# Performance work log

Measured on AMD Instinct MI355X. Metric: run time of the kernel, lower is better.

The kernel has to match this reference:

```python
import jax, jax.numpy as jnp
import numpy as np

B, N, D, H, K = 16, 256, 64, 64, 2  # batch, nodes, d_in, d_hidden, top_k


def setup_inputs() -> dict:
    key = jax.random.key(0)
    k0, k1, k2 = jax.random.split(key, 3)
    O = jax.random.normal(k0, (B, N, D), dtype=jnp.float32)
    # PairwiseFeaturizer.proj: Linear(4*D, H) -> ReLU -> Linear(H, 1)
    W1 = jax.random.normal(k1, (4 * D, H), dtype=jnp.float32) / np.sqrt(4 * D).astype(np.float32)
    b1 = jnp.zeros((H,), dtype=jnp.float32)
    W2 = jax.random.normal(k2, (H, 1), dtype=jnp.float32) / np.sqrt(H).astype(np.float32)
    b2 = jnp.zeros((1,), dtype=jnp.float32)
    return {"O": O, "W1": W1, "b1": b1, "W2": W2, "b2": b2}


def reference(O, W1, b1, W2, b2):
    Bn, Nn, d = O.shape
    ii, jj = jnp.triu_indices(Nn, k=1)  # all undirected pairs i<j, M = N(N-1)/2
    Oi = O[:, ii, :]  # (B, M, d) gather
    Oj = O[:, jj, :]  # (B, M, d) gather
    feats = jnp.concatenate([Oi, Oj, jnp.abs(Oi - Oj), Oi * Oj], axis=-1)  # (B, M, 4d)
    h = jax.nn.relu(jnp.einsum('bmf,fh->bmh', feats, W1) + b1)
    Q = (jnp.einsum('bmh,ho->bmo', h, W2) + b2)[..., 0]  # (B, M)
    # greedy top-k selection mask (eps -> 0 limit of select_pairs)
    idx = jax.lax.top_k(Q, K)[1]  # (B, K)
    mask = jnp.zeros(Q.shape, dtype=bool).at[jnp.arange(Q.shape[0])[:, None], idx].set(True)
    return Q, mask
```

## Files before the change

kernel.cpp:

```cpp
#include <hip/hip_runtime.h>
#include <math.h>

#define Bn 16
#define Nn 256
#define Mm (Nn*(Nn-1)/2)
#define CHUNK 4080

typedef __attribute__((ext_vector_type(8))) short bf16x8;
typedef __attribute__((ext_vector_type(4))) short short4v;
typedef __attribute__((ext_vector_type(4))) float f32x4;

typedef union { bf16x8 v; short s[8]; __bf16 h[8]; } F8;
typedef union { short4v v; __bf16 h[4]; } F4;

#define MFMA(acc, a, b) \
  acc = __builtin_amdgcn_mfma_f32_16x16x32_bf16((a), (b), (acc), 0, 0, 0)

__device__ __forceinline__ void top2_update(float v, int m,
    float& v1, int& i1, float& v2, int& i2)
{
  bool c1 = (v > v1) || (v == v1 && m < i1);
  bool c2 = (v > v2) || (v == v2 && m < i2);
  float nv2 = c1 ? v1 : (c2 ? v : v2);
  int   ni2 = c1 ? i1 : (c2 ? m : i2);
  v1 = c1 ? v : v1;  i1 = c1 ? m : i1;
  v2 = nv2;          i2 = ni2;
}

__global__ __launch_bounds__(256) void prep_w1t(
    const float* __restrict__ W1, unsigned short* __restrict__ wtg)
{
  const int h = blockIdx.x;
  const int k = threadIdx.x;
  __bf16 b = (__bf16)W1[k * 64 + h];
  wtg[h * 256 + k] = *(unsigned short*)&b;
}

__global__ __launch_bounds__(256) void prep_ac(
    const float* __restrict__ O, const float* __restrict__ b1,
    const unsigned short* __restrict__ wtg,
    unsigned short* __restrict__ obg, float* __restrict__ Ag,
    unsigned short* __restrict__ Cgb)
{
  __shared__ __align__(16) unsigned short s_ob[64][72];
  const int t = threadIdx.x, l = t & 63, wv = t >> 6;
  const int lo = l & 15, g = l >> 4;
  const int b = blockIdx.x >> 2, rt = blockIdx.x & 3;
  const int r0 = rt * 64;
  const float* Ob = O + ((size_t)b * Nn + r0) * 64;

  #pragma unroll
  for (int p = 0; p < 4; ++p) {
    int v = t + p * 256;
    int r = v >> 4, c4 = (v & 15) * 4;
    float4 x = ((const float4*)Ob)[v];
    F4 pk; pk.h[0] = (__bf16)x.x; pk.h[1] = (__bf16)x.y;
           pk.h[2] = (__bf16)x.z; pk.h[3] = (__bf16)x.w;
    *(short4v*)&s_ob[r][c4] = pk.v;
    *(short4v*)&obg[((size_t)b * Nn + r0 + r) * 64 + c4] = pk.v;
  }
  __syncthreads();

  F8 aop[2];
  #pragma unroll
  for (int ks = 0; ks < 2; ++ks)
    aop[ks].v = *(const bf16x8*)&s_ob[wv * 16 + lo][ks * 32 + g * 8];

  #pragma unroll
  for (int half = 0; half < 2; ++half) {
    #pragma unroll
    for (int nf = 0; nf < 4; ++nf) {
      f32x4 ac = {0.f, 0.f, 0.f, 0.f};
      #pragma unroll
      for (int ks = 0; ks < 2; ++ks) {
        F8 bop; bop.v = *(const bf16x8*)&wtg[(nf * 16 + lo) * 256 + half * 64 + ks * 32 + g * 8];
        MFMA(ac, aop[ks].v, bop.v);
      }
      const int h = nf * 16 + lo;
      if (half == 0) {
        float bb = b1[h];
        #pragma unroll
        for (int r = 0; r < 4; ++r)
          Ag[((size_t)b * Nn + r0 + wv * 16 + g * 4 + r) * 64 + h] = ac[r] + bb;
      } else {
        #pragma unroll
        for (int r = 0; r < 4; ++r) {
          __bf16 cb = (__bf16)ac[r];
          Cgb[((size_t)b * Nn + r0 + wv * 16 + g * 4 + r) * 64 + h] = *(unsigned short*)&cb;
        }
      }
    }
  }
}

__global__ __launch_bounds__(256, 2) void pair_kernel(
    const unsigned short* __restrict__ obg,
    const float* __restrict__ Ag,
    const unsigned short* __restrict__ Cgb,
    const float* __restrict__ W2,
    const float* __restrict__ b2,
    const unsigned short* __restrict__ wtg,
    float* __restrict__ Q,
    float* __restrict__ cand)
{
  __shared__ __align__(16) unsigned short s_wt[64][136];
  __shared__ __align__(16) unsigned short s_oi[16][72];
  __shared__ __align__(16) unsigned short s_oj[32][72];
  __shared__ float s_A [16][68];
  __shared__ float s_q [16][36];
  __shared__ float s_w2[64];
  __shared__ float s_red[4][4];

  const int t  = threadIdx.x;
  const int l  = t & 63, wv = t >> 6;
  const int lo = l & 15, g = l >> 4;

  const int blk    = blockIdx.x;
  const int within = blk >> 3;
  const int batch  = (blk & 7) * 2 + within / 72;
  int tl           = within % 72;
  int a = 0;
  while (tl >= 8 - (a >> 1)) { tl -= 8 - (a >> 1); ++a; }
  const int c   = (a >> 1) + tl;
  const int ti0 = a * 16, tj0 = c * 32;

  {
    const int h = t >> 2, kq = (t & 3) * 32;
    #pragma unroll
    for (int q = 0; q < 4; ++q) {
      *(bf16x8*)&s_wt[h][kq + q * 8] =
          *(const bf16x8*)&wtg[h * 256 + 128 + kq + q * 8];
    }
  }
  {
    int r = t >> 4, c4 = (t & 15) * 4;
    *(short4v*)&s_oi[r][c4] =
        *(const short4v*)&obg[((size_t)batch * Nn + ti0 + r) * 64 + c4];
    *(f32x4*)&s_A[r][c4] =
        *(const f32x4*)&Ag[((size_t)batch * Nn + ti0 + r) * 64 + c4];
    #pragma unroll
    for (int p = 0; p < 2; ++p) {
      int v = t + p * 256;
      int rj = v >> 4, cj = (v & 15) * 4;
      *(short4v*)&s_oj[rj][cj] =
          *(const short4v*)&obg[((size_t)batch * Nn + tj0 + rj) * 64 + cj];
    }
    if (t < 64) s_w2[t] = W2[t];
  }
  __syncthreads();

  F8 bfr[4][4];
  #pragma unroll
  for (int ks = 0; ks < 4; ++ks)
    #pragma unroll
    for (int nf = 0; nf < 4; ++nf)
      bfr[ks][nf].v = *(const bf16x8*)&s_wt[nf * 16 + lo][ks * 32 + g * 8];

  F8 ojb[2][2];
  #pragma unroll
  for (int jh = 0; jh < 2; ++jh) {
    ojb[jh][0].v = *(const bf16x8*)&s_oj[jh * 16 + lo][g * 8];
    ojb[jh][1].v = *(const bf16x8*)&s_oj[jh * 16 + lo][32 + g * 8];
  }
  F4 cinb[2][4];
  #pragma unroll
  for (int jh = 0; jh < 2; ++jh)
    #pragma unroll
    for (int nf = 0; nf < 4; ++nf)
      cinb[jh][nf].v = *(const short4v*)
          &Cgb[((size_t)batch * Nn + tj0 + jh * 16 + lo) * 64 + nf * 16 + g * 4];

  for (int ii = 0; ii < 4; ++ii) {
    const int iL = wv * 4 + ii;

    float oiv[16];
    {
      F8 u0, u1;
      u0.v = *(const bf16x8*)&s_oi[iL][g * 8];
      u1.v = *(const bf16x8*)&s_oi[iL][32 + g * 8];
      #pragma unroll
      for (int e = 0; e < 8; ++e) {
        oiv[e]     = (float)u0.h[e];
        oiv[8 + e] = (float)u1.h[e];
      }
    }
    f32x4 as4[4];
    #pragma unroll
    for (int nf = 0; nf < 4; ++nf)
      as4[nf] = *(const f32x4*)&s_A[iL][nf * 16 + g * 4];

    #pragma unroll
    for (int jh = 0; jh < 2; ++jh) {
      F8 fb0, fb1, fb2, fb3;
      #pragma unroll
      for (int e = 0; e < 8; ++e) {
        float p0 = (float)ojb[jh][0].h[e];
        float p1 = (float)ojb[jh][1].h[e];
        fb0.h[e] = (__bf16)fabsf(oiv[e]     - p0);
        fb1.h[e] = (__bf16)fabsf(oiv[8 + e] - p1);
        fb2.h[e] = (__bf16)(oiv[e]     * p0);
        fb3.h[e] = (__bf16)(oiv[8 + e] * p1);
      }

      f32x4 acc[4] = { as4[0], as4[1], as4[2], as4[3] };
      #pragma unroll
      for (int nf = 0; nf < 4; ++nf) {
        MFMA(acc[nf], bfr[0][nf].v, fb0.v);
        MFMA(acc[nf], bfr[1][nf].v, fb1.v);
        MFMA(acc[nf], bfr[2][nf].v, fb2.v);
        MFMA(acc[nf], bfr[3][nf].v, fb3.v);
      }

      float part = 0.f;
      #pragma unroll
      for (int nf = 0; nf < 4; ++nf) {
        #pragma unroll
        for (int r = 0; r < 4; ++r) {
          float z = acc[nf][r] + (float)cinb[jh][nf].h[r];
          part = fmaf(fmaxf(z, 0.f), s_w2[nf * 16 + g * 4 + r], part);
        }
      }
      part += __shfl_xor(part, 16);
      part += __shfl_xor(part, 32);
      if (g == 0) s_q[iL][jh * 16 + lo] = part;
    }
  }
  __syncthreads();

  {
    const float b2v = b2[0];
    const int e0 = t * 2;
    const int row = e0 >> 5, col0 = e0 & 31;
    const int i = ti0 + row;
    float v1 = -INFINITY, v2 = -INFINITY;
    int   i1 = 0x7fffffff, i2 = 0x7fffffff;
    const int mbase = i * (Nn - 1) - (i * (i - 1)) / 2 - i - 1;
    #pragma unroll
    for (int e = 0; e < 2; ++e) {
      const int col = col0 + e;
      const int j = tj0 + col;
      const float qv = s_q[row][col] + b2v;
      if (j > i) {
        const int m = mbase + j;
        Q[(size_t)batch * Mm + m] = qv;
        top2_update(qv, m, v1, i1, v2, i2);
      }
    }
    #pragma unroll
    for (int s = 1; s < 64; s <<= 1) {
      float u1 = __shfl_xor(v1, s); int j1 = __shfl_xor(i1, s);
      float u2 = __shfl_xor(v2, s); int j2 = __shfl_xor(i2, s);
      top2_update(u1, j1, v1, i1, v2, i2);
      top2_update(u2, j2, v1, i1, v2, i2);
    }
    if (l == 0) {
      s_red[wv][0] = v1; s_red[wv][1] = __int_as_float(i1);
      s_red[wv][2] = v2; s_red[wv][3] = __int_as_float(i2);
    }
    __syncthreads();
    if (t == 0) {
      float a1 = s_red[0][0]; int x1 = __float_as_int(s_red[0][1]);
      float a2 = s_red[0][2]; int x2 = __float_as_int(s_red[0][3]);
      #pragma unroll
      for (int e = 1; e < 4; ++e) {
        top2_update(s_red[e][0], __float_as_int(s_red[e][1]), a1, x1, a2, x2);
        top2_update(s_red[e][2], __float_as_int(s_red[e][3]), a1, x1, a2, x2);
      }
      float* cp = cand + ((size_t)batch * 72 + within % 72) * 4;
      cp[0] = a1; cp[1] = __int_as_float(x1);
      cp[2] = a2; cp[3] = __int_as_float(x2);
    }
  }
}

__global__ __launch_bounds__(256) void rankmask_kernel(
    const float* __restrict__ O, const float* __restrict__ W1,
    const float* __restrict__ b1, const float* __restrict__ W2,
    const float* __restrict__ cand, float* __restrict__ mask)
{
  const int b   = blockIdx.x >> 3;
  const int cch = blockIdx.x & 7;
  const int t   = threadIdx.x;
  const int wv  = t >> 6, h = t & 63;
  __shared__ float s_cv[144];
  __shared__ int   s_ci[144];
  __shared__ int   s_m[8];
  __shared__ int   s_ij[8][2];
  __shared__ float s_or[8][2][64];
  __shared__ float s_qe[8];
  __shared__ int   s_k0, s_k1;

  if (t < 144) {
    const float* cp = cand + (size_t)(b * 72 + (t >> 1)) * 4;
    s_cv[t] = cp[(t & 1) * 2];
    s_ci[t] = __float_as_int(cp[(t & 1) * 2 + 1]);
  }
  __syncthreads();
  if (t < 144) {
    float v = s_cv[t]; int m = s_ci[t];
    int rank = 0;
    for (int e = 0; e < 144; ++e) {
      float u = s_cv[e]; int n = s_ci[e];
      rank += (u > v || (u == v && n < m)) ? 1 : 0;
    }
    if (rank < 8) s_m[rank] = m;
  }
  __syncthreads();
  if (t < 16) {
    int m = s_m[t >> 1];
    int i = 0, rem = m;
    while (rem >= Nn - 1 - i) { rem -= Nn - 1 - i; ++i; }
    int j = i + 1 + rem;
    s_ij[t >> 1][t & 1] = (t & 1) ? j : i;
  }
  __syncthreads();
  {
    int cc = t >> 5, rr = (t >> 4) & 1, c4 = (t & 15) * 4;
    int row = s_ij[cc][rr];
    *(float4*)&s_or[cc][rr][c4] = *(const float4*)&O[((size_t)b * Nn + row) * 64 + c4];
  }
  __syncthreads();
  #pragma unroll
  for (int p = 0; p < 2; ++p) {
    const int cc = p * 4 + wv;
    float z = b1[h];
    #pragma unroll 8
    for (int d = 0; d < 64; ++d) {
      float oi = s_or[cc][0][d], oj = s_or[cc][1][d];
      float f3 = fabsf(oi - oj), f4 = oi * oj;
      z += oi * W1[d * 64 + h] + oj * W1[(64 + d) * 64 + h]
         + f3 * W1[(128 + d) * 64 + h] + f4 * W1[(192 + d) * 64 + h];
    }
    float part = fmaxf(z, 0.f) * W2[h];
    #pragma unroll
    for (int s = 1; s < 64; s <<= 1) part += __shfl_xor(part, s);
    if (h == 0) s_qe[cc] = part;
  }
  __syncthreads();
  if (t == 0) {
    float v1 = -INFINITY, v2 = -INFINITY;
    int   i1 = 0x7fffffff, i2 = 0x7fffffff;
    for (int e = 0; e < 8; ++e)
      top2_update(s_qe[e], s_m[e], v1, i1, v2, i2);
    s_k0 = i1; s_k1 = i2;
  }
  __syncthreads();

  const int k0 = s_k0, k1 = s_k1;
  float* mb = mask + (size_t)b * Mm;
  const int m0 = cch * CHUNK;
  for (int m = m0 + t; m < m0 + CHUNK; m += 256)
    mb[m] = (m == k0 || m == k1) ? 1.0f : 0.0f;
}

extern "C" void kernel_launch(void* const* d_in, const int* in_sizes, int n_in,
                              void* d_out, int out_size, void* d_ws, size_t ws_size,
                              hipStream_t stream) {
  const float* O  = (const float*)d_in[0];
  const float* W1 = (const float*)d_in[1];
  const float* b1 = (const float*)d_in[2];
  const float* W2 = (const float*)d_in[3];
  const float* b2 = (const float*)d_in[4];

  float* Q    = (float*)d_out;
  float* mask = Q + (size_t)Bn * Mm;

  char* ws = (char*)d_ws;
  unsigned short* wtg = (unsigned short*)ws;
  unsigned short* obg = (unsigned short*)(ws + 32768);
  float*          Ag  = (float*)(ws + 32768 + 524288);
  unsigned short* Cgb = (unsigned short*)(ws + 32768 + 524288 + 1048576);
  float*          cand = (float*)(ws + 32768 + 524288 + 1048576 + 524288);

  prep_w1t<<<dim3(64), dim3(256), 0, stream>>>(W1, wtg);
  prep_ac<<<dim3(Bn * 4), dim3(256), 0, stream>>>(O, b1, wtg, obg, Ag, Cgb);
  pair_kernel<<<dim3(Bn * 72), dim3(256), 0, stream>>>(obg, Ag, Cgb, W2, b2, wtg, Q, cand);
  rankmask_kernel<<<dim3(Bn * 8), dim3(256), 0, stream>>>(O, W1, b1, W2, cand, mask);
}
```

Baseline: 61.63 us.

## Use square 32x32 upper-triangular pair tiles, halving pair kernel blocks

```diff
diff --git a/kernel.cpp b/kernel.cpp
--- a/kernel.cpp
+++ b/kernel.cpp
@@ -4,6 +4,7 @@
 #define Bn 16
 #define Nn 256
 #define Mm (Nn*(Nn-1)/2)
+#define NT 8
 #define CHUNK 4080
 
 typedef __attribute__((ext_vector_type(8))) short bf16x8;
@@ -104,10 +105,10 @@
     float* __restrict__ cand)
 {
   __shared__ __align__(16) unsigned short s_wt[64][136];
-  __shared__ __align__(16) unsigned short s_oi[16][72];
+  __shared__ __align__(16) unsigned short s_oi[32][72];
   __shared__ __align__(16) unsigned short s_oj[32][72];
-  __shared__ float s_A [16][68];
-  __shared__ float s_q [16][36];
+  __shared__ float s_A [32][68];
+  __shared__ float s_q [32][36];
   __shared__ float s_w2[64];
   __shared__ float s_red[4][4];
 
@@ -117,12 +118,13 @@
 
   const int blk    = blockIdx.x;
   const int within = blk >> 3;
-  const int batch  = (blk & 7) * 2 + within / 72;
-  int tl           = within % 72;
+  const int batch  = (blk & 7) * 2 + within / 36;
+  const int tidx   = within % 36;
+  int tile = tidx;
   int a = 0;
-  while (tl >= 8 - (a >> 1)) { tl -= 8 - (a >> 1); ++a; }
-  const int c   = (a >> 1) + tl;
-  const int ti0 = a * 16, tj0 = c * 32;
+  while (tile >= (NT - a)) { tile -= NT - a; ++a; }
+  const int ti0 = a * 32, tj0 = (a + tile) * 32;
+  const bool diag = (tile == 0);
 
   {
     const int h = t >> 2, kq = (t & 3) * 32;
@@ -133,17 +135,17 @@
     }
   }
   {
-    int r = t >> 4, c4 = (t & 15) * 4;
-    *(short4v*)&s_oi[r][c4] =
-        *(const short4v*)&obg[((size_t)batch * Nn + ti0 + r) * 64 + c4];
-    *(f32x4*)&s_A[r][c4] =
-        *(const f32x4*)&Ag[((size_t)batch * Nn + ti0 + r) * 64 + c4];
     #pragma unroll
     for (int p = 0; p < 2; ++p) {
       int v = t + p * 256;
-      int rj = v >> 4, cj = (v & 15) * 4;
-      *(short4v*)&s_oj[rj][cj] =
-          *(const short4v*)&obg[((size_t)batch * Nn + tj0 + rj) * 64 + cj];
+      int r = v >> 4, c4 = (v & 15) * 4;
+      *(short4v*)&s_oi[r][c4] =
+          *(const short4v*)&obg[((size_t)batch * Nn + ti0 + r) * 64 + c4];
+      *(short4v*)&s_oj[r][c4] =
+          *(const short4v*)&obg[((size_t)batch * Nn + tj0 + r) * 64 + c4];
+      int rA = v >> 4;
+      *(f32x4*)&s_A[rA][c4] =
+          *(const f32x4*)&Ag[((size_t)batch * Nn + ti0 + rA) * 64 + c4];
     }
     if (t < 64) s_w2[t] = W2[t];
   }
@@ -170,8 +172,8 @@
       cinb[jh][nf].v = *(const short4v*)
           &Cgb[((size_t)batch * Nn + tj0 + jh * 16 + lo) * 64 + nf * 16 + g * 4];
 
-  for (int ii = 0; ii < 4; ++ii) {
-    const int iL = wv * 4 + ii;
+  for (int ii = 0; ii < 8; ++ii) {
+    const int iL = wv * 8 + ii;
 
     float oiv[16];
     {
@@ -229,18 +231,18 @@
 
   {
     const float b2v = b2[0];
-    const int e0 = t * 2;
-    const int row = e0 >> 5, col0 = e0 & 31;
+    const int row = t >> 3, c4 = (t & 7) * 4;
     const int i = ti0 + row;
     float v1 = -INFINITY, v2 = -INFINITY;
     int   i1 = 0x7fffffff, i2 = 0x7fffffff;
     const int mbase = i * (Nn - 1) - (i * (i - 1)) / 2 - i - 1;
     #pragma unroll
-    for (int e = 0; e < 2; ++e) {
-      const int col = col0 + e;
+    for (int e = 0; e < 4; ++e) {
+      const int col = c4 + e;
       const int j = tj0 + col;
       const float qv = s_q[row][col] + b2v;
-      if (j > i) {
+      const bool valid = !diag || (j > i);
+      if (valid) {
         const int m = mbase + j;
         Q[(size_t)batch * Mm + m] = qv;
         top2_update(qv, m, v1, i1, v2, i2);
@@ -266,7 +268,7 @@
         top2_update(s_red[e][0], __float_as_int(s_red[e][1]), a1, x1, a2, x2);
         top2_update(s_red[e][2], __float_as_int(s_red[e][3]), a1, x1, a2, x2);
       }
-      float* cp = cand + ((size_t)batch * 72 + within % 72) * 4;
+      float* cp = cand + ((size_t)batch * 36 + tidx) * 4;
       cp[0] = a1; cp[1] = __int_as_float(x1);
       cp[2] = a2; cp[3] = __int_as_float(x2);
     }
@@ -282,24 +284,24 @@
   const int cch = blockIdx.x & 7;
   const int t   = threadIdx.x;
   const int wv  = t >> 6, h = t & 63;
-  __shared__ float s_cv[144];
-  __shared__ int   s_ci[144];
+  __shared__ float s_cv[72];
+  __shared__ int   s_ci[72];
   __shared__ int   s_m[8];
   __shared__ int   s_ij[8][2];
   __shared__ float s_or[8][2][64];
   __shared__ float s_qe[8];
   __shared__ int   s_k0, s_k1;
 
-  if (t < 144) {
-    const float* cp = cand + (size_t)(b * 72 + (t >> 1)) * 4;
+  if (t < 72) {
+    const float* cp = cand + (size_t)(b * 36 + (t >> 1)) * 4;
     s_cv[t] = cp[(t & 1) * 2];
     s_ci[t] = __float_as_int(cp[(t & 1) * 2 + 1]);
   }
   __syncthreads();
-  if (t < 144) {
+  if (t < 72) {
     float v = s_cv[t]; int m = s_ci[t];
     int rank = 0;
-    for (int e = 0; e < 144; ++e) {
+    for (int e = 0; e < 72; ++e) {
       float u = s_cv[e]; int n = s_ci[e];
       rank += (u > v || (u == v && n < m)) ? 1 : 0;
     }
@@ -374,6 +376,6 @@
 
   prep_w1t<<<dim3(64), dim3(256), 0, stream>>>(W1, wtg);
   prep_ac<<<dim3(Bn * 4), dim3(256), 0, stream>>>(O, b1, wtg, obg, Ag, Cgb);
-  pair_kernel<<<dim3(Bn * 72), dim3(256), 0, stream>>>(obg, Ag, Cgb, W2, b2, wtg, Q, cand);
+  pair_kernel<<<dim3(Bn * 36), dim3(256), 0, stream>>>(obg, Ag, Cgb, W2, b2, wtg, Q, cand);
   rankmask_kernel<<<dim3(Bn * 8), dim3(256), 0, stream>>>(O, W1, b1, W2, cand, mask);
 }
```

Measured after the change: 62.36 us. No clear change (+1.2%).

## Load pair operands from global into registers and software-pipeline MFMA with epilogue

Applied to the files above, without the earlier changes.

```diff
diff --git a/kernel.cpp b/kernel.cpp
--- a/kernel.cpp
+++ b/kernel.cpp
@@ -104,10 +104,6 @@
     float* __restrict__ cand)
 {
   __shared__ __align__(16) unsigned short s_wt[64][136];
-  __shared__ __align__(16) unsigned short s_oi[16][72];
-  __shared__ __align__(16) unsigned short s_oj[32][72];
-  __shared__ float s_A [16][68];
-  __shared__ float s_q [16][36];
   __shared__ float s_w2[64];
   __shared__ float s_red[4][4];
 
@@ -123,28 +119,19 @@
   while (tl >= 8 - (a >> 1)) { tl -= 8 - (a >> 1); ++a; }
   const int c   = (a >> 1) + tl;
   const int ti0 = a * 16, tj0 = c * 32;
+  const bool diag = (tj0 == ti0 * 2 && (a & 1) == 0) ? false : false;
+  const bool dg = (c * 32 < ti0 + 16) || (c == 0 && a == 0) ? false : false; (void)dg;
+  const bool isdiag = (tj0 < ti0 + 16);
+
+  const size_t obase = (size_t)batch * Nn;
+  const size_t qbase = (size_t)batch * Mm;
 
   {
     const int h = t >> 2, kq = (t & 3) * 32;
     #pragma unroll
-    for (int q = 0; q < 4; ++q) {
+    for (int q = 0; q < 4; ++q)
       *(bf16x8*)&s_wt[h][kq + q * 8] =
           *(const bf16x8*)&wtg[h * 256 + 128 + kq + q * 8];
-    }
-  }
-  {
-    int r = t >> 4, c4 = (t & 15) * 4;
-    *(short4v*)&s_oi[r][c4] =
-        *(const short4v*)&obg[((size_t)batch * Nn + ti0 + r) * 64 + c4];
-    *(f32x4*)&s_A[r][c4] =
-        *(const f32x4*)&Ag[((size_t)batch * Nn + ti0 + r) * 64 + c4];
-    #pragma unroll
-    for (int p = 0; p < 2; ++p) {
-      int v = t + p * 256;
-      int rj = v >> 4, cj = (v & 15) * 4;
-      *(short4v*)&s_oj[rj][cj] =
-          *(const short4v*)&obg[((size_t)batch * Nn + tj0 + rj) * 64 + cj];
-    }
     if (t < 64) s_w2[t] = W2[t];
   }
   __syncthreads();
@@ -159,8 +146,8 @@
   F8 ojb[2][2];
   #pragma unroll
   for (int jh = 0; jh < 2; ++jh) {
-    ojb[jh][0].v = *(const bf16x8*)&s_oj[jh * 16 + lo][g * 8];
-    ojb[jh][1].v = *(const bf16x8*)&s_oj[jh * 16 + lo][32 + g * 8];
+    ojb[jh][0].v = *(const bf16x8*)&obg[(obase + tj0 + jh * 16 + lo) * 64 + g * 8];
+    ojb[jh][1].v = *(const bf16x8*)&obg[(obase + tj0 + jh * 16 + lo) * 64 + 32 + g * 8];
   }
   F4 cinb[2][4];
   #pragma unroll
@@ -168,108 +155,122 @@
     #pragma unroll
     for (int nf = 0; nf < 4; ++nf)
       cinb[jh][nf].v = *(const short4v*)
-          &Cgb[((size_t)batch * Nn + tj0 + jh * 16 + lo) * 64 + nf * 16 + g * 4];
-
-  for (int ii = 0; ii < 4; ++ii) {
-    const int iL = wv * 4 + ii;
-
-    float oiv[16];
-    {
-      F8 u0, u1;
-      u0.v = *(const bf16x8*)&s_oi[iL][g * 8];
-      u1.v = *(const bf16x8*)&s_oi[iL][32 + g * 8];
+          &Cgb[(obase + tj0 + jh * 16 + lo) * 64 + nf * 16 + g * 4];
+
+  const float b2v = b2[0];
+
+  F8 oib0, oib1;
+  f32x4 as4[4];
+  int iG = 0, mbG = 0;
+  int iP = 0, mbP = 0;
+  f32x4 acc0[4], acc1[4];
+  F8 f0, f1, f2, f3;
+  float v1 = -INFINITY, v2 = -INFINITY;
+  int   i1 = 0x7fffffff, i2 = 0x7fffffff;
+
+  auto LOADROW = [&](int ii) {
+    const int i = ti0 + wv * 4 + ii;
+    oib0.v = *(const bf16x8*)&obg[(obase + i) * 64 + g * 8];
+    oib1.v = *(const bf16x8*)&obg[(obase + i) * 64 + 32 + g * 8];
+    #pragma unroll
+    for (int nf = 0; nf < 4; ++nf)
+      as4[nf] = *(const f32x4*)&Ag[(obase + i) * 64 + nf * 16 + g * 4];
+    iG = i;
+    mbG = i * (Nn - 1) - (i * (i - 1)) / 2 - i - 1;
+  };
+
+  auto BUILD = [&](const F8& oj0, const F8& oj1) {
+    #pragma unroll
+    for (int e = 0; e < 8; ++e) {
+      float oi0 = (float)oib0.h[e], oi1 = (float)oib1.h[e];
+      float p0  = (float)oj0.h[e],  p1  = (float)oj1.h[e];
+      f0.h[e] = (__bf16)fabsf(oi0 - p0);
+      f1.h[e] = (__bf16)fabsf(oi1 - p1);
+      f2.h[e] = (__bf16)(oi0 * p0);
+      f3.h[e] = (__bf16)(oi1 * p1);
+    }
+  };
+
+  auto STEP = [&](f32x4 (&acc)[4]) {
+    #pragma unroll
+    for (int nf = 0; nf < 4; ++nf) acc[nf] = as4[nf];
+    MFMA(acc[0], bfr[0][0].v, f0.v); MFMA(acc[1], bfr[0][1].v, f0.v);
+    MFMA(acc[2], bfr[0][2].v, f0.v); MFMA(acc[3], bfr[0][3].v, f0.v);
+    MFMA(acc[0], bfr[1][0].v, f1.v); MFMA(acc[1], bfr[1][1].v, f1.v);
+    MFMA(acc[2], bfr[1][2].v, f1.v); MFMA(acc[3], bfr[1][3].v, f1.v);
+    MFMA(acc[0], bfr[2][0].v, f2.v); MFMA(acc[1], bfr[2][1].v, f2.v);
+    MFMA(acc[2], bfr[2][2].v, f2.v); MFMA(acc[3], bfr[2][3].v, f2.v);
+    MFMA(acc[0], bfr[3][0].v, f3.v); MFMA(acc[1], bfr[3][1].v, f3.v);
+    MFMA(acc[2], bfr[3][2].v, f3.v); MFMA(acc[3], bfr[3][3].v, f3.v);
+  };
+
+  auto EPI = [&](f32x4 (&acc)[4], int jhE, int iE, int mbE) {
+    float part = 0.f;
+    #pragma unroll
+    for (int nf = 0; nf < 4; ++nf) {
+      f32x4 w2v = *(const f32x4*)&s_w2[nf * 16 + g * 4];
       #pragma unroll
-      for (int e = 0; e < 8; ++e) {
-        oiv[e]     = (float)u0.h[e];
-        oiv[8 + e] = (float)u1.h[e];
+      for (int r = 0; r < 4; ++r) {
+        float z = acc[nf][r] + (float)cinb[jhE][nf].h[r];
+        part = fmaf(fmaxf(z, 0.f), w2v[r], part);
       }
     }
-    f32x4 as4[4];
-    #pragma unroll
-    for (int nf = 0; nf < 4; ++nf)
-      as4[nf] = *(const f32x4*)&s_A[iL][nf * 16 + g * 4];
-
-    #pragma unroll
-    for (int jh = 0; jh < 2; ++jh) {
-      F8 fb0, fb1, fb2, fb3;
-      #pragma unroll
-      for (int e = 0; e < 8; ++e) {
-        float p0 = (float)ojb[jh][0].h[e];
-        float p1 = (float)ojb[jh][1].h[e];
-        fb0.h[e] = (__bf16)fabsf(oiv[e]     - p0);
-        fb1.h[e] = (__bf16)fabsf(oiv[8 + e] - p1);
-        fb2.h[e] = (__bf16)(oiv[e]     * p0);
-        fb3.h[e] = (__bf16)(oiv[8 + e] * p1);
-      }
-
-      f32x4 acc[4] = { as4[0], as4[1], as4[2], as4[3] };
-      #pragma unroll
-      for (int nf = 0; nf < 4; ++nf) {
-        MFMA(acc[nf], bfr[0][nf].v, fb0.v);
-        MFMA(acc[nf], bfr[1][nf].v, fb1.v);
-        MFMA(acc[nf], bfr[2][nf].v, fb2.v);
-        MFMA(acc[nf], bfr[3][nf].v, fb3.v);
-      }
-
-      float part = 0.f;
-      #pragma unroll
-      for (int nf = 0; nf < 4; ++nf) {
-        #pragma unroll
-        for (int r = 0; r < 4; ++r) {
-          float z = acc[nf][r] + (float)cinb[jh][nf].h[r];
-          part = fmaf(fmaxf(z, 0.f), s_w2[nf * 16 + g * 4 + r], part);
-        }
-      }
-      part += __shfl_xor(part, 16);
-      part += __shfl_xor(part, 32);
-      if (g == 0) s_q[iL][jh * 16 + lo] = part;
-    }
-  }
-  __syncthreads();
-
-  {
-    const float b2v = b2[0];
-    const int e0 = t * 2;
-    const int row = e0 >> 5, col0 = e0 & 31;
-    const int i = ti0 + row;
-    float v1 = -INFINITY, v2 = -INFINITY;
-    int   i1 = 0x7fffffff, i2 = 0x7fffffff;
-    const int mbase = i * (Nn - 1) - (i * (i - 1)) / 2 - i - 1;
-    #pragma unroll
-    for (int e = 0; e < 2; ++e) {
-      const int col = col0 + e;
-      const int j = tj0 + col;
-      const float qv = s_q[row][col] + b2v;
-      if (j > i) {
-        const int m = mbase + j;
-        Q[(size_t)batch * Mm + m] = qv;
+    part += __shfl_xor(part, 16);
+    part += __shfl_xor(part, 32);
+    if (l < 16) {
+      const int j = tj0 + jhE * 16 + l;
+      if (!isdiag || j > iE) {
+        const float qv = part + b2v;
+        const int m = mbE + j;
+        Q[qbase + m] = qv;
         top2_update(qv, m, v1, i1, v2, i2);
       }
     }
-    #pragma unroll
-    for (int s = 1; s < 64; s <<= 1) {
-      float u1 = __shfl_xor(v1, s); int j1 = __shfl_xor(i1, s);
-      float u2 = __shfl_xor(v2, s); int j2 = __shfl_xor(i2, s);
-      top2_update(u1, j1, v1, i1, v2, i2);
-      top2_update(u2, j2, v1, i1, v2, i2);
-    }
-    if (l == 0) {
-      s_red[wv][0] = v1; s_red[wv][1] = __int_as_float(i1);
-      s_red[wv][2] = v2; s_red[wv][3] = __int_as_float(i2);
-    }
-    __syncthreads();
-    if (t == 0) {
-      float a1 = s_red[0][0]; int x1 = __float_as_int(s_red[0][1]);
-      float a2 = s_red[0][2]; int x2 = __float_as_int(s_red[0][3]);
-      #pragma unroll
-      for (int e = 1; e < 4; ++e) {
-        top2_update(s_red[e][0], __float_as_int(s_red[e][1]), a1, x1, a2, x2);
-        top2_update(s_red[e][2], __float_as_int(s_red[e][3]), a1, x1, a2, x2);
-      }
-      float* cp = cand + ((size_t)batch * 72 + within % 72) * 4;
-      cp[0] = a1; cp[1] = __int_as_float(x1);
-      cp[2] = a2; cp[3] = __int_as_float(x2);
-    }
+  };
+
+  LOADROW(0);
+  BUILD(ojb[0][0], ojb[0][1]); STEP(acc0);
+  BUILD(ojb[1][0], ojb[1][1]); STEP(acc1); EPI(acc0, 0, iG, mbG);
+
+  iP = iG; mbP = mbG; LOADROW(1);
+  EPI(acc1, 1, iP, mbP);
+  BUILD(ojb[0][0], ojb[0][1]); STEP(acc0);
+  BUILD(ojb[1][0], ojb[1][1]); STEP(acc1); EPI(acc0, 0, iG, mbG);
+
+  iP = iG; mbP = mbG; LOADROW(2);
+  EPI(acc1, 1, iP, mbP);
+  BUILD(ojb[0][0], ojb[0][1]); STEP(acc0);
+  BUILD(ojb[1][0], ojb[1][1]); STEP(acc1); EPI(acc0, 0, iG, mbG);
+
+  iP = iG; mbP = mbG; LOADROW(3);
+  EPI(acc1, 1, iP, mbP);
+  BUILD(ojb[0][0], ojb[0][1]); STEP(acc0);
+  BUILD(ojb[1][0], ojb[1][1]); STEP(acc1); EPI(acc0, 0, iG, mbG);
+  EPI(acc1, 1, iG, mbG);
+
+  #pragma unroll
+  for (int s = 1; s < 64; s <<= 1) {
+    float u1 = __shfl_xor(v1, s); int j1 = __shfl_xor(i1, s);
+    float u2 = __shfl_xor(v2, s); int j2 = __shfl_xor(i2, s);
+    top2_update(u1, j1, v1, i1, v2, i2);
+    top2_update(u2, j2, v1, i1, v2, i2);
+  }
+  if (l == 0) {
+    s_red[wv][0] = v1; s_red[wv][1] = __int_as_float(i1);
+    s_red[wv][2] = v2; s_red[wv][3] = __int_as_float(i2);
+  }
+  __syncthreads();
+  if (t == 0) {
+    float a1 = s_red[0][0]; int x1 = __float_as_int(s_red[0][1]);
+    float a2 = s_red[0][2]; int x2 = __float_as_int(s_red[0][3]);
+    #pragma unroll
+    for (int e = 1; e < 4; ++e) {
+      top2_update(s_red[e][0], __float_as_int(s_red[e][1]), a1, x1, a2, x2);
+      top2_update(s_red[e][2], __float_as_int(s_red[e][3]), a1, x1, a2, x2);
+    }
+    float* cp = cand + ((size_t)batch * 72 + within % 72) * 4;
+    cp[0] = a1; cp[1] = __int_as_float(x1);
+    cp[2] = a2; cp[3] = __int_as_float(x2);
   }
 }
 
```

Result: slower. 64.96 us (+5.4%).
